# Kernel tuning notes

Hardware: AMD Instinct MI355X
Metric: run time of the kernel (lower is better)

Reference implementation:

```python
import jax, jax.numpy as jnp
import numpy as np

TOP_K = 2  # config.moe_config['moe_top_k']


def setup_inputs() -> dict:
    key = jax.random.key(0)
    k1, k2, k3, k4 = jax.random.split(key, 4)
    B, S, H, F, E = 2, 1024, 1024, 2048, 8
    def init(k, shape, fan_in):
        return jax.random.normal(k, shape, jnp.float32) / np.float32(np.sqrt(fan_in))
    return {
        "hidden_states": jax.random.normal(k1, (B, S, H), jnp.float32),
        "router_w": init(k2, (H, E), H),          # Linear(hidden, E, bias=False)
        "W1": init(k3, (E, H, 2 * F), H),          # per-expert Linear(hidden, 2*ffn)
        "W2": init(k4, (E, F, H), F),              # per-expert Linear(ffn, hidden)
    }


def reference(hidden_states, router_w, W1, W2):
    B, S, H = hidden_states.shape
    E = router_w.shape[1]
    x = hidden_states.reshape(-1, H)                      # [N, H], N = B*S
    N = x.shape[0]

    # router: logits -> fp32 softmax -> top-k -> renormalize (matches torch)
    logits = x @ router_w                                  # [N, E]
    probs = jax.nn.softmax(logits.astype(jnp.float32), axis=-1)
    rw, sel = jax.lax.top_k(probs, TOP_K)                  # [N, k]
    rw = rw / rw.sum(axis=-1, keepdims=True)
    rw = rw.astype(x.dtype)

    # combine weights per (token, expert); top-k experts are distinct so add==set
    cw = jnp.zeros((N, E), x.dtype).at[jnp.arange(N)[:, None], sel].add(rw)

    # per-expert SwiGLU MLP over all tokens, masked combine (full-capacity MoE)
    h = jnp.einsum('nh,ehf->enf', x, W1)                   # [E, N, 2F]
    a, b = jnp.split(h, 2, axis=-1)                        # gate, value halves
    g = jax.nn.silu(a) * b                                 # [E, N, F]
    y = jnp.einsum('enf,efh->enh', g, W2)                  # [E, N, H]
    out = jnp.einsum('enh,ne->nh', y, cw)                  # weighted scatter-combine
    return out.reshape(B, S, H)
```

## Files before the change

kernel.cpp:

```cpp
#include <hip/hip_runtime.h>
#include <hip/hip_bf16.h>

#define H_DIM 1024
#define E_NUM 8
#define F_DIM 2048
#define N_TOK 2048
typedef unsigned int uint;
typedef short bf16x8 __attribute__((ext_vector_type(8)));
typedef float f32x4 __attribute__((ext_vector_type(4)));

#define WS_CNT   0
#define WS_LIST  256
#define WS_W     (WS_LIST + 8*N_TOK*4)
#define WS_G     131072
#define WS_Y     (WS_G + 4096*2048*2)
#define WS_XB    WS_Y


static __device__ __forceinline__ uint f2bf(float f) {
    uint u = __builtin_bit_cast(uint, f);
    return (u + 0x7FFFu + ((u >> 16) & 1u)) >> 16;
}
static __device__ __forceinline__ float bflo(uint u) { return __builtin_bit_cast(float, u << 16); }
static __device__ __forceinline__ float bfhi(uint u) { return __builtin_bit_cast(float, u & 0xFFFF0000u); }
static __device__ __forceinline__ uint cvtpk(float a, float b) {
    uint r;
    asm("v_cvt_pk_bf16_f32 %0, %1, %2" : "=v"(r) : "v"(a), "v"(b));
    return r;
}
static __device__ __forceinline__ void gload_lds16(const void* g, void* l) {
    __builtin_amdgcn_global_load_lds(
        (const __attribute__((address_space(1))) unsigned int*)g,
        (__attribute__((address_space(3))) unsigned int*)l,
        16, 0, 0);
}

__global__ __launch_bounds__(256) void cvt_x_kernel(const float* __restrict__ x,
                                                    unsigned short* __restrict__ xb)
{
    int c = blockIdx.x * 256 + threadIdx.x;
    int row = c >> 7, b = c & 127;
    int t = b >> 3, s = b & 7;
    int klo = t*64 + (s >> 2)*32 + (s & 3)*4;
    const float* xr = x + (size_t)row * H_DIM;
    float4 lo = *(const float4*)(xr + klo);
    float4 hi = *(const float4*)(xr + klo + 16);
    uint4 o;
    o.x = cvtpk(lo.x, lo.y); o.y = cvtpk(lo.z, lo.w);
    o.z = cvtpk(hi.x, hi.y); o.w = cvtpk(hi.z, hi.w);
    *(uint4*)(xb + (size_t)row * H_DIM + b*8) = o;
}

__global__ __launch_bounds__(256) void router_kernel(
    const float* __restrict__ x, const float* __restrict__ rw,
    int* __restrict__ cnt, int* __restrict__ list, float* __restrict__ w_entry)
{
    int wave = threadIdx.x >> 6, lane = threadIdx.x & 63;
    int n = blockIdx.x * 4 + wave;
    const float* xr = x + (size_t)n * H_DIM;
    float acc[8] = {0,0,0,0,0,0,0,0};
    #pragma unroll
    for (int i = 0; i < H_DIM/64; ++i) {
        int h = i*64 + lane;
        float xv = xr[h];
        const float4* rr = (const float4*)(rw + (size_t)h*8);
        float4 r0 = rr[0], r1 = rr[1];
        acc[0] += xv*r0.x; acc[1] += xv*r0.y; acc[2] += xv*r0.z; acc[3] += xv*r0.w;
        acc[4] += xv*r1.x; acc[5] += xv*r1.y; acc[6] += xv*r1.z; acc[7] += xv*r1.w;
    }
    #pragma unroll
    for (int e = 0; e < 8; ++e) {
        float v = acc[e];
        #pragma unroll
        for (int off = 32; off; off >>= 1) v += __shfl_xor(v, off);
        acc[e] = v;
    }
    int e0 = 0;
    #pragma unroll
    for (int e = 1; e < 8; ++e) if (acc[e] > acc[e0]) e0 = e;
    int e1 = -1;
    #pragma unroll
    for (int e = 0; e < 8; ++e) if (e != e0 && (e1 < 0 || acc[e] > acc[e1])) e1 = e;
    float w0 = 1.0f / (1.0f + __expf(acc[e1] - acc[e0]));
    float w1 = 1.0f - w0;
    if (lane == 0) {
        int p0 = atomicAdd(&cnt[e0], 1);
        list[e0*N_TOK + p0] = n*2;
        w_entry[n*2] = w0;
        int p1 = atomicAdd(&cnt[e1], 1);
        list[e1*N_TOK + p1] = n*2 + 1;
        w_entry[n*2+1] = w1;
    }
}

template<int IS_G1>
__global__ __launch_bounds__(256, 4) void moe_gemm_kernel(
    const unsigned short* __restrict__ Asrc, const float* __restrict__ W,
    const int* __restrict__ cnt, const int* __restrict__ list,
    const float* __restrict__ w_entry, unsigned short* __restrict__ dst)
{
    constexpr int KTOT  = IS_G1 ? H_DIM : F_DIM;
    constexpr int BLD   = IS_G1 ? 2*F_DIM : H_DIM;
    constexpr int DLD   = IS_G1 ? F_DIM : H_DIM;
    constexpr int ALD   = IS_G1 ? H_DIM : F_DIM;
    constexpr int NMT   = 32;
    constexpr int NNT   = IS_G1 ? 32 : 16;
    constexpr int BSROW = IS_G1 ? 512 : 256;
    constexpr int NBS   = IS_G1 ? 4 : 2;
    constexpr int NM    = IS_G1 ? 4 : 2;
    constexpr int NT    = KTOT / 64;

    __shared__ __align__(16) unsigned short As[2][64*64];
    __shared__ __align__(16) uint Bs[32*BSROW/4];
    __shared__ int   s_entry[64];
    __shared__ float s_wrow[64];

    constexpr int nb = NMT * NNT * E_NUM;
    constexpr int chunk = nb >> 3;
    int bid = blockIdx.x;
    int f  = (bid & 7) * chunk + (bid >> 3);
    int mt = f % NMT;
    int nt = (f / NMT) % NNT;
    int e  = f / (NMT * NNT);

    const int c = cnt[e];
    if (mt * 64 >= c) return;
    const int tid = threadIdx.x;

    if (tid < 64) {
        int r = mt*64 + tid;
        int rr = r < c ? r : c - 1;
        int ent = list[e*N_TOK + rr];
        s_entry[tid] = ent;
        if constexpr (!IS_G1) s_wrow[tid] = w_entry[ent];
    }
    __syncthreads();

    const int lane = tid & 63, wid = tid >> 6;
    const int l15 = lane & 15, lg = lane >> 4;
    const int wr = IS_G1 ? 0 : (wid >> 1);
    const int wc = wid & 1;
    const int rowbase = IS_G1 ? 0 : wr*32;

    const unsigned short* a_src[2];
    #pragma unroll
    for (int i = 0; i < 2; ++i) {
        int sl  = wid*2048 + i*1024 + lane*16;
        int row = sl >> 7;
        int kb  = ((sl >> 4) & 7) ^ (row & 7);
        int ent = s_entry[row];
        int arow = IS_G1 ? (ent >> 1) : ent;
        a_src[i] = Asrc + (size_t)arow * ALD + kb*8;
    }

    const float* Wb = W + (size_t)e * (size_t)(IS_G1 ? H_DIM*2*F_DIM : F_DIM*H_DIM);
    const float* b_src[NBS]; int b_dst[NBS];
    #pragma unroll
    for (int s = 0; s < NBS; ++s) {
        int q = tid + s*256;
        int kp, c4, gc;
        if constexpr (IS_G1) {
            kp = q >> 5; c4 = q & 31;
            gc = (c4 < 16) ? (nt*64 + 4*c4) : (F_DIM + nt*64 + 4*(c4-16));
        } else {
            kp = q >> 4; c4 = q & 15;
            gc = nt*64 + 4*c4;
        }
        b_src[s] = Wb + (size_t)(2*kp) * BLD + gc;
        b_dst[s] = (kp*BSROW + c4*16) ^ ((kp & 4) << 4);
    }

    int a_addr[NM][2];
    #pragma unroll
    for (int m = 0; m < NM; ++m)
        #pragma unroll
        for (int kk = 0; kk < 2; ++kk) {
            int row = rowbase + m*16 + l15;
            a_addr[m][kk] = row*128 + ((kk*64 + lg*16) ^ ((row & 7) << 4));
        }
    int b_base[2][2];
    const int xorv = ((2*lg) & 4) << 4;
    #pragma unroll
    for (int j = 0; j < 2; ++j) {
        int cb = IS_G1 ? (j ? (4 + wid) : wid) : (wc*2 + j);
        int co = ((cb*16 + l15) * 4) ^ xorv;
        #pragma unroll
        for (int kk = 0; kk < 2; ++kk)
            b_base[j][kk] = (kk*16 + 2*lg)*BSROW + co;
    }

    f32x4 acc[NM][2];
    #pragma unroll
    for (int m = 0; m < NM; ++m)
        #pragma unroll
        for (int j = 0; j < 2; ++j) acc[m][j] = (f32x4){0.f,0.f,0.f,0.f};

    auto compute_step = [&](const char* ab) {
        #pragma unroll
        for (int kk = 0; kk < 2; ++kk) {
            bf16x8 af[NM];
            #pragma unroll
            for (int m = 0; m < NM; ++m)
                af[m] = *(const bf16x8*)(ab + a_addr[m][kk]);
            bf16x8 bfr[2];
            #pragma unroll
            for (int j = 0; j < 2; ++j) {
                const char* bb = (const char*)Bs + b_base[j][kk];
                union { uint u[4]; bf16x8 v; } bu;
                bu.u[0] = *(const uint*)(bb);
                bu.u[1] = *(const uint*)(bb + BSROW);
                bu.u[2] = *(const uint*)(bb + 8*BSROW);
                bu.u[3] = *(const uint*)(bb + 9*BSROW);
                bfr[j] = bu.v;
            }
            #pragma unroll
            for (int m = 0; m < NM; ++m)
                #pragma unroll
                for (int j = 0; j < 2; ++j)
                    acc[m][j] = __builtin_amdgcn_mfma_f32_16x16x32_bf16(af[m], bfr[j], acc[m][j], 0, 0, 0);
        }
    };

    #pragma unroll
    for (int i = 0; i < 2; ++i)
        gload_lds16(a_src[i], (char*)As[0] + wid*2048 + i*1024);
    {
        float4 r0[NBS], r1[NBS];
        #pragma unroll
        for (int s = 0; s < NBS; ++s) {
            r0[s] = *(const float4*)(b_src[s]);
            r1[s] = *(const float4*)(b_src[s] + BLD);
        }
        #pragma unroll
        for (int s = 0; s < NBS; ++s) {
            uint4 w4;
            w4.x = cvtpk(r0[s].x, r1[s].x); w4.y = cvtpk(r0[s].y, r1[s].y);
            w4.z = cvtpk(r0[s].z, r1[s].z); w4.w = cvtpk(r0[s].w, r1[s].w);
            *(uint4*)((char*)Bs + b_dst[s]) = w4;
        }
    }
    __syncthreads();

    for (int t = 0; t < NT; ++t) {
        float4 r0[NBS], r1[NBS];
        const bool more = (t + 1 < NT);
        if (more) {
            #pragma unroll
            for (int i = 0; i < 2; ++i)
                gload_lds16(a_src[i] + (t+1)*64, (char*)As[(t+1) & 1] + wid*2048 + i*1024);
            #pragma unroll
            for (int s = 0; s < NBS; ++s) {
                const float* b0 = b_src[s] + (size_t)(t+1) * 64 * BLD;
                r0[s] = *(const float4*)b0;
                r1[s] = *(const float4*)(b0 + BLD);
            }
        }
        compute_step((const char*)As[t & 1]);
        __syncthreads();
        if (more) {
            #pragma unroll
            for (int s = 0; s < NBS; ++s) {
                uint4 w4;
                w4.x = cvtpk(r0[s].x, r1[s].x); w4.y = cvtpk(r0[s].y, r1[s].y);
                w4.z = cvtpk(r0[s].z, r1[s].z); w4.w = cvtpk(r0[s].w, r1[s].w);
                *(uint4*)((char*)Bs + b_dst[s]) = w4;
            }
            __syncthreads();
        }
    }

    if constexpr (IS_G1) {
        const int pbase = nt*64 + ((wid >> 1)*4 + (l15 >> 2))*8 + (wid & 1)*4 + (l15 & 3);
        #pragma unroll
        for (int m = 0; m < NM; ++m) {
            f32x4 ga = acc[m][0], gv = acc[m][1];
            #pragma unroll
            for (int i = 0; i < 4; ++i) {
                int rl = m*16 + lg*4 + i;
                if (mt*64 + rl < c) {
                    int ent = s_entry[rl];
                    float a = ga[i];
                    float g = (a / (1.f + __expf(-a))) * gv[i];
                    dst[(size_t)ent * DLD + pbase] = (unsigned short)f2bf(g);
                }
            }
        }
    } else {
        #pragma unroll
        for (int m = 0; m < NM; ++m)
            #pragma unroll
            for (int j = 0; j < 2; ++j) {
                #pragma unroll
                for (int i = 0; i < 4; ++i) {
                    int rl = rowbase + m*16 + lg*4 + i;
                    if (mt*64 + rl < c) {
                        int ent = s_entry[rl];
                        float v = s_wrow[rl] * acc[m][j][i];
                        int col = nt*64 + wc*32 + j*16 + l15;
                        dst[(size_t)ent * DLD + col] = (unsigned short)f2bf(v);
                    }
                }
            }
    }
}

__global__ __launch_bounds__(256) void combine_kernel(
    const unsigned short* __restrict__ y, float* __restrict__ out)
{
    int gid = blockIdx.x * 256 + threadIdx.x;
    size_t base = (size_t)gid * 8;
    int n = (int)(base >> 10), h = (int)(base & 1023);
    const uint4 a = *(const uint4*)(y + (size_t)(2*n)   * 1024 + h);
    const uint4 b = *(const uint4*)(y + (size_t)(2*n+1) * 1024 + h);
    float4 o0, o1;
    o0.x = bflo(a.x)+bflo(b.x); o0.y = bfhi(a.x)+bfhi(b.x);
    o0.z = bflo(a.y)+bflo(b.y); o0.w = bfhi(a.y)+bfhi(b.y);
    o1.x = bflo(a.z)+bflo(b.z); o1.y = bfhi(a.z)+bfhi(b.z);
    o1.z = bflo(a.w)+bflo(b.w); o1.w = bfhi(a.w)+bfhi(b.w);
    *(float4*)(out + base)     = o0;
    *(float4*)(out + base + 4) = o1;
}

extern "C" void kernel_launch(void* const* d_in, const int* in_sizes, int n_in,
                              void* d_out, int out_size, void* d_ws, size_t ws_size,
                              hipStream_t stream) {
    const float* x  = (const float*)d_in[0];
    const float* rw = (const float*)d_in[1];
    const float* W1 = (const float*)d_in[2];
    const float* W2 = (const float*)d_in[3];
    float* out = (float*)d_out;
    char* ws = (char*)d_ws;
    int*   cnt     = (int*)(ws + WS_CNT);
    int*   list    = (int*)(ws + WS_LIST);
    float* w_entry = (float*)(ws + WS_W);
    unsigned short* g  = (unsigned short*)(ws + WS_G);
    unsigned short* y  = (unsigned short*)(ws + WS_Y);
    unsigned short* xb = (unsigned short*)(ws + WS_XB);

    hipMemsetAsync(cnt, 0, E_NUM * sizeof(int), stream);
    cvt_x_kernel<<<N_TOK*H_DIM/2048, 256, 0, stream>>>(x, xb);
    router_kernel<<<N_TOK/4, 256, 0, stream>>>(x, rw, cnt, list, w_entry);
    moe_gemm_kernel<1><<<32*32*E_NUM, 256, 0, stream>>>(xb, W1, cnt, list, w_entry, g);
    moe_gemm_kernel<0><<<32*16*E_NUM, 256, 0, stream>>>(g,  W2, cnt, list, w_entry, y);
    combine_kernel<<<(out_size/8 + 255)/256, 256, 0, stream>>>(y, out);
}
```

Measured before the change: 207.5 us.

## Stream fp32 weights directly into LDS with async loads and double-buffer both operands

The MoE GEMM kernel now loads fp32 weight tiles straight into LDS through global_load_lds and converts them to bf16 at fragment-read time, replacing the register round-trip and the separate LDS store. Both the A and B tiles are double-buffered with a two-stage prefetch, and explicit vmcnt waits plus barriers replace the per-iteration syncthreads pairs. The second GEMM is reshaped to 64x128 tiles so both GEMMs share one 4-wave layout, and the token list and weights are read from global memory instead of being staged in shared memory. LDS use grows and occupancy is lowered to 2 blocks per SM. The weight conversion is also repeated on every fragment read instead of once per tile.

```diff
diff --git a/kernel.cpp b/kernel.cpp
--- a/kernel.cpp
+++ b/kernel.cpp
@@ -33,6 +33,10 @@
         (const __attribute__((address_space(1))) unsigned int*)g,
         (__attribute__((address_space(3))) unsigned int*)l,
         16, 0, 0);
+}
+template<int N> static __device__ __forceinline__ void vmwait() {
+    if constexpr (N == 0)       asm volatile("s_waitcnt vmcnt(0)" ::: "memory");
+    else if constexpr (N == 10) asm volatile("s_waitcnt vmcnt(10)" ::: "memory");
 }
 
 __global__ __launch_bounds__(256) void cvt_x_kernel(const float* __restrict__ x,
@@ -94,7 +98,7 @@
 }
 
 template<int IS_G1>
-__global__ __launch_bounds__(256, 4) void moe_gemm_kernel(
+__global__ __launch_bounds__(256, 2) void moe_gemm_kernel(
     const unsigned short* __restrict__ Asrc, const float* __restrict__ W,
     const int* __restrict__ cnt, const int* __restrict__ list,
     const float* __restrict__ w_entry, unsigned short* __restrict__ dst)
@@ -104,16 +108,11 @@
     constexpr int DLD   = IS_G1 ? F_DIM : H_DIM;
     constexpr int ALD   = IS_G1 ? H_DIM : F_DIM;
     constexpr int NMT   = 32;
-    constexpr int NNT   = IS_G1 ? 32 : 16;
-    constexpr int BSROW = IS_G1 ? 512 : 256;
-    constexpr int NBS   = IS_G1 ? 4 : 2;
-    constexpr int NM    = IS_G1 ? 4 : 2;
+    constexpr int NNT   = IS_G1 ? 32 : 8;
     constexpr int NT    = KTOT / 64;
 
     __shared__ __align__(16) unsigned short As[2][64*64];
-    __shared__ __align__(16) uint Bs[32*BSROW/4];
-    __shared__ int   s_entry[64];
-    __shared__ float s_wrow[64];
+    __shared__ __align__(16) uint Bs[2][64*128];
 
     constexpr int nb = NMT * NNT * E_NUM;
     constexpr int chunk = nb >> 3;
@@ -126,21 +125,9 @@
     const int c = cnt[e];
     if (mt * 64 >= c) return;
     const int tid = threadIdx.x;
-
-    if (tid < 64) {
-        int r = mt*64 + tid;
-        int rr = r < c ? r : c - 1;
-        int ent = list[e*N_TOK + rr];
-        s_entry[tid] = ent;
-        if constexpr (!IS_G1) s_wrow[tid] = w_entry[ent];
-    }
-    __syncthreads();
-
     const int lane = tid & 63, wid = tid >> 6;
     const int l15 = lane & 15, lg = lane >> 4;
-    const int wr = IS_G1 ? 0 : (wid >> 1);
-    const int wc = wid & 1;
-    const int rowbase = IS_G1 ? 0 : wr*32;
+    const int lbase = e * N_TOK + mt * 64;
 
     const unsigned short* a_src[2];
     #pragma unroll
@@ -148,137 +135,118 @@
         int sl  = wid*2048 + i*1024 + lane*16;
         int row = sl >> 7;
         int kb  = ((sl >> 4) & 7) ^ (row & 7);
-        int ent = s_entry[row];
+        int rr  = (mt*64 + row) < c ? row : (c - 1 - mt*64);
+        int ent = list[lbase + rr];
         int arow = IS_G1 ? (ent >> 1) : ent;
         a_src[i] = Asrc + (size_t)arow * ALD + kb*8;
     }
 
     const float* Wb = W + (size_t)e * (size_t)(IS_G1 ? H_DIM*2*F_DIM : F_DIM*H_DIM);
-    const float* b_src[NBS]; int b_dst[NBS];
-    #pragma unroll
-    for (int s = 0; s < NBS; ++s) {
-        int q = tid + s*256;
-        int kp, c4, gc;
-        if constexpr (IS_G1) {
-            kp = q >> 5; c4 = q & 31;
-            gc = (c4 < 16) ? (nt*64 + 4*c4) : (F_DIM + nt*64 + 4*(c4-16));
-        } else {
-            kp = q >> 4; c4 = q & 15;
-            gc = nt*64 + 4*c4;
-        }
-        b_src[s] = Wb + (size_t)(2*kp) * BLD + gc;
-        b_dst[s] = (kp*BSROW + c4*16) ^ ((kp & 4) << 4);
-    }
-
-    int a_addr[NM][2];
-    #pragma unroll
-    for (int m = 0; m < NM; ++m)
+    const float* b_srcp[8];
+    #pragma unroll
+    for (int i = 0; i < 8; ++i) {
+        int k  = wid*16 + i*2 + (lane >> 5);
+        int c4 = (lane & 31) ^ (k & 12);
+        int gc;
+        if constexpr (IS_G1) gc = (c4 < 16) ? (nt*64 + 4*c4) : (F_DIM + nt*64 + 4*(c4-16));
+        else                 gc = nt*128 + 4*c4;
+        b_srcp[i] = Wb + (size_t)k * BLD + gc;
+    }
+
+    int a_addr[4][2];
+    #pragma unroll
+    for (int m = 0; m < 4; ++m)
         #pragma unroll
         for (int kk = 0; kk < 2; ++kk) {
-            int row = rowbase + m*16 + l15;
+            int row = m*16 + l15;
             a_addr[m][kk] = row*128 + ((kk*64 + lg*16) ^ ((row & 7) << 4));
         }
-    int b_base[2][2];
-    const int xorv = ((2*lg) & 4) << 4;
+    int b_base[2];
     #pragma unroll
     for (int j = 0; j < 2; ++j) {
-        int cb = IS_G1 ? (j ? (4 + wid) : wid) : (wc*2 + j);
-        int co = ((cb*16 + l15) * 4) ^ xorv;
-        #pragma unroll
-        for (int kk = 0; kk < 2; ++kk)
-            b_base[j][kk] = (kk*16 + 2*lg)*BSROW + co;
-    }
-
-    f32x4 acc[NM][2];
-    #pragma unroll
-    for (int m = 0; m < NM; ++m)
+        int cb = j ? (4 + wid) : wid;
+        b_base[j] = ((cb*16 + l15) * 4) ^ (lg << 6);
+    }
+
+    f32x4 acc[4][2];
+    #pragma unroll
+    for (int m = 0; m < 4; ++m)
         #pragma unroll
         for (int j = 0; j < 2; ++j) acc[m][j] = (f32x4){0.f,0.f,0.f,0.f};
 
-    auto compute_step = [&](const char* ab) {
+    auto STAGE = [&](int tt) {
+        const int b = tt & 1;
+        #pragma unroll
+        for (int i = 0; i < 2; ++i)
+            gload_lds16(a_src[i] + tt*64, (char*)As[b] + wid*2048 + i*1024);
+        #pragma unroll
+        for (int i = 0; i < 8; ++i)
+            gload_lds16(b_srcp[i] + (size_t)tt * 64 * BLD, (char*)Bs[b] + wid*8192 + i*1024);
+    };
+
+    auto compute_step = [&](const char* ab, const char* bb0) {
         #pragma unroll
         for (int kk = 0; kk < 2; ++kk) {
-            bf16x8 af[NM];
-            #pragma unroll
-            for (int m = 0; m < NM; ++m)
+            bf16x8 af[4];
+            #pragma unroll
+            for (int m = 0; m < 4; ++m)
                 af[m] = *(const bf16x8*)(ab + a_addr[m][kk]);
             bf16x8 bfr[2];
             #pragma unroll
             for (int j = 0; j < 2; ++j) {
-                const char* bb = (const char*)Bs + b_base[j][kk];
+                const char* bb = bb0 + (kk*32 + 4*lg)*512 + b_base[j];
+                float fA0 = *(const float*)(bb);
+                float fA1 = *(const float*)(bb + 512);
+                float fA2 = *(const float*)(bb + 1024);
+                float fA3 = *(const float*)(bb + 1536);
+                float fB0 = *(const float*)(bb + 8192);
+                float fB1 = *(const float*)(bb + 8192 + 512);
+                float fB2 = *(const float*)(bb + 8192 + 1024);
+                float fB3 = *(const float*)(bb + 8192 + 1536);
                 union { uint u[4]; bf16x8 v; } bu;
-                bu.u[0] = *(const uint*)(bb);
-                bu.u[1] = *(const uint*)(bb + BSROW);
-                bu.u[2] = *(const uint*)(bb + 8*BSROW);
-                bu.u[3] = *(const uint*)(bb + 9*BSROW);
+                bu.u[0] = cvtpk(fA0, fA1);
+                bu.u[1] = cvtpk(fA2, fA3);
+                bu.u[2] = cvtpk(fB0, fB1);
+                bu.u[3] = cvtpk(fB2, fB3);
                 bfr[j] = bu.v;
             }
             #pragma unroll
-            for (int m = 0; m < NM; ++m)
+            for (int m = 0; m < 4; ++m)
                 #pragma unroll
                 for (int j = 0; j < 2; ++j)
                     acc[m][j] = __builtin_amdgcn_mfma_f32_16x16x32_bf16(af[m], bfr[j], acc[m][j], 0, 0, 0);
         }
     };
 
-    #pragma unroll
-    for (int i = 0; i < 2; ++i)
-        gload_lds16(a_src[i], (char*)As[0] + wid*2048 + i*1024);
-    {
-        float4 r0[NBS], r1[NBS];
-        #pragma unroll
-        for (int s = 0; s < NBS; ++s) {
-            r0[s] = *(const float4*)(b_src[s]);
-            r1[s] = *(const float4*)(b_src[s] + BLD);
-        }
-        #pragma unroll
-        for (int s = 0; s < NBS; ++s) {
-            uint4 w4;
-            w4.x = cvtpk(r0[s].x, r1[s].x); w4.y = cvtpk(r0[s].y, r1[s].y);
-            w4.z = cvtpk(r0[s].z, r1[s].z); w4.w = cvtpk(r0[s].w, r1[s].w);
-            *(uint4*)((char*)Bs + b_dst[s]) = w4;
-        }
-    }
-    __syncthreads();
-
+    STAGE(0);
+    STAGE(1);
+
+    #pragma unroll
     for (int t = 0; t < NT; ++t) {
-        float4 r0[NBS], r1[NBS];
-        const bool more = (t + 1 < NT);
-        if (more) {
-            #pragma unroll
-            for (int i = 0; i < 2; ++i)
-                gload_lds16(a_src[i] + (t+1)*64, (char*)As[(t+1) & 1] + wid*2048 + i*1024);
-            #pragma unroll
-            for (int s = 0; s < NBS; ++s) {
-                const float* b0 = b_src[s] + (size_t)(t+1) * 64 * BLD;
-                r0[s] = *(const float4*)b0;
-                r1[s] = *(const float4*)(b0 + BLD);
-            }
-        }
-        compute_step((const char*)As[t & 1]);
-        __syncthreads();
-        if (more) {
-            #pragma unroll
-            for (int s = 0; s < NBS; ++s) {
-                uint4 w4;
-                w4.x = cvtpk(r0[s].x, r1[s].x); w4.y = cvtpk(r0[s].y, r1[s].y);
-                w4.z = cvtpk(r0[s].z, r1[s].z); w4.w = cvtpk(r0[s].w, r1[s].w);
-                *(uint4*)((char*)Bs + b_dst[s]) = w4;
-            }
-            __syncthreads();
+        if (t < NT - 1) vmwait<10>();
+        else            vmwait<0>();
+        __builtin_amdgcn_sched_barrier(0);
+        __builtin_amdgcn_s_barrier();
+        asm volatile("" ::: "memory");
+        compute_step((const char*)As[t & 1], (const char*)Bs[t & 1]);
+        if (t + 2 < NT) {
+            asm volatile("" ::: "memory");
+            __builtin_amdgcn_s_barrier();
+            asm volatile("" ::: "memory");
+            STAGE(t + 2);
         }
     }
 
     if constexpr (IS_G1) {
         const int pbase = nt*64 + ((wid >> 1)*4 + (l15 >> 2))*8 + (wid & 1)*4 + (l15 & 3);
         #pragma unroll
-        for (int m = 0; m < NM; ++m) {
+        for (int m = 0; m < 4; ++m) {
             f32x4 ga = acc[m][0], gv = acc[m][1];
             #pragma unroll
             for (int i = 0; i < 4; ++i) {
                 int rl = m*16 + lg*4 + i;
                 if (mt*64 + rl < c) {
-                    int ent = s_entry[rl];
+                    int ent = list[lbase + rl];
                     float a = ga[i];
                     float g = (a / (1.f + __expf(-a))) * gv[i];
                     dst[(size_t)ent * DLD + pbase] = (unsigned short)f2bf(g);
@@ -287,17 +255,17 @@
         }
     } else {
         #pragma unroll
-        for (int m = 0; m < NM; ++m)
-            #pragma unroll
-            for (int j = 0; j < 2; ++j) {
-                #pragma unroll
-                for (int i = 0; i < 4; ++i) {
-                    int rl = rowbase + m*16 + lg*4 + i;
-                    if (mt*64 + rl < c) {
-                        int ent = s_entry[rl];
-                        float v = s_wrow[rl] * acc[m][j][i];
-                        int col = nt*64 + wc*32 + j*16 + l15;
-                        dst[(size_t)ent * DLD + col] = (unsigned short)f2bf(v);
+        for (int m = 0; m < 4; ++m)
+            #pragma unroll
+            for (int i = 0; i < 4; ++i) {
+                int rl = m*16 + lg*4 + i;
+                if (mt*64 + rl < c) {
+                    int ent = list[lbase + rl];
+                    float w = w_entry[ent];
+                    #pragma unroll
+                    for (int j = 0; j < 2; ++j) {
+                        int col = nt*128 + (j ? (64 + wid*16) : (wid*16)) + l15;
+                        dst[(size_t)ent * DLD + col] = (unsigned short)f2bf(w * acc[m][j][i]);
                     }
                 }
             }
@@ -341,6 +309,6 @@
     cvt_x_kernel<<<N_TOK*H_DIM/2048, 256, 0, stream>>>(x, xb);
     router_kernel<<<N_TOK/4, 256, 0, stream>>>(x, rw, cnt, list, w_entry);
     moe_gemm_kernel<1><<<32*32*E_NUM, 256, 0, stream>>>(xb, W1, cnt, list, w_entry, g);
-    moe_gemm_kernel<0><<<32*16*E_NUM, 256, 0, stream>>>(g,  W2, cnt, list, w_entry, y);
+    moe_gemm_kernel<0><<<32*8*E_NUM, 256, 0, stream>>>(g,  W2, cnt, list, w_entry, y);
     combine_kernel<<<(out_size/8 + 255)/256, 256, 0, stream>>>(y, out);
 }
```

Result: slower. 254.2 us (+22.5%).

## Gather routed tokens contiguously and double-buffer weight tiles in MoE GEMMs

Applied to the files above, without the earlier changes.

Replaces the dense x-to-bf16 conversion with a prefix-sum plus gather kernel that writes each expert's routed tokens contiguously in bf16. The GEMMs then read A rows directly instead of going through an index indirection, and the G1 output is stored in that expert-sorted order. The main loop is rebuilt with double-buffered 32-row B sub-tiles in LDS, explicit vmcnt/lgkmcnt waits and barriers, to overlap global weight loads with MFMA work. It also raises the G2 occupancy hint and looks up the routing weights per row in the epilogue. The cost is two extra small kernel launches and a more fragile hand-written wait schedule.

```diff
diff --git a/kernel.cpp b/kernel.cpp
--- a/kernel.cpp
+++ b/kernel.cpp
@@ -10,11 +10,12 @@
 typedef float f32x4 __attribute__((ext_vector_type(4)));
 
 #define WS_CNT   0
+#define WS_OFF   64
 #define WS_LIST  256
 #define WS_W     (WS_LIST + 8*N_TOK*4)
 #define WS_G     131072
-#define WS_Y     (WS_G + 4096*2048*2)
-#define WS_XB    WS_Y
+#define WS_AX    (WS_G + 4096*2048*2)
+#define WS_Y     WS_AX
 
 
 static __device__ __forceinline__ uint f2bf(float f) {
@@ -34,21 +35,16 @@
         (__attribute__((address_space(3))) unsigned int*)l,
         16, 0, 0);
 }
-
-__global__ __launch_bounds__(256) void cvt_x_kernel(const float* __restrict__ x,
-                                                    unsigned short* __restrict__ xb)
-{
-    int c = blockIdx.x * 256 + threadIdx.x;
-    int row = c >> 7, b = c & 127;
-    int t = b >> 3, s = b & 7;
-    int klo = t*64 + (s >> 2)*32 + (s & 3)*4;
-    const float* xr = x + (size_t)row * H_DIM;
-    float4 lo = *(const float4*)(xr + klo);
-    float4 hi = *(const float4*)(xr + klo + 16);
-    uint4 o;
-    o.x = cvtpk(lo.x, lo.y); o.y = cvtpk(lo.z, lo.w);
-    o.z = cvtpk(hi.x, hi.y); o.w = cvtpk(hi.z, hi.w);
-    *(uint4*)(xb + (size_t)row * H_DIM + b*8) = o;
+template<int N> static __device__ __forceinline__ void vmwait() {
+    if constexpr (N == 0)      asm volatile("s_waitcnt vmcnt(0)" ::: "memory");
+    else if constexpr (N == 2) asm volatile("s_waitcnt vmcnt(2)" ::: "memory");
+    else if constexpr (N == 4) asm volatile("s_waitcnt vmcnt(4)" ::: "memory");
+}
+static __device__ __forceinline__ void lgk0_bar() {
+    asm volatile("s_waitcnt lgkmcnt(0)" ::: "memory");
+    __builtin_amdgcn_sched_barrier(0);
+    __builtin_amdgcn_s_barrier();
+    asm volatile("" ::: "memory");
 }
 
 __global__ __launch_bounds__(256) void router_kernel(
@@ -93,27 +89,61 @@
     }
 }
 
+__global__ void prefix_kernel(const int* __restrict__ cnt, int* __restrict__ off) {
+    if (threadIdx.x == 0) {
+        int s = 0;
+        #pragma unroll
+        for (int e = 0; e < E_NUM; ++e) { off[e] = s; s += cnt[e]; }
+        off[E_NUM] = s;
+    }
+}
+
+__global__ __launch_bounds__(256) void gather_kernel(
+    const float* __restrict__ x, const int* __restrict__ cnt, const int* __restrict__ off,
+    const int* __restrict__ list, unsigned short* __restrict__ Ax)
+{
+    int e = blockIdx.x >> 9;
+    int r = (blockIdx.x & 511)*4 + (threadIdx.x >> 6);
+    int lane = threadIdx.x & 63;
+    if (r >= cnt[e]) return;
+    int ent = list[e*N_TOK + r];
+    const float* xr = x + (size_t)(ent >> 1) * H_DIM;
+    unsigned short* dr = Ax + (size_t)(off[e] + r) * H_DIM;
+    #pragma unroll
+    for (int q = 0; q < 2; ++q) {
+        int b = lane*2 + q;
+        int t = b >> 3, s = b & 7;
+        int klo = t*64 + (s >> 2)*32 + (s & 3)*4;
+        float4 lo = *(const float4*)(xr + klo);
+        float4 hi = *(const float4*)(xr + klo + 16);
+        uint4 o;
+        o.x = cvtpk(lo.x, lo.y); o.y = cvtpk(lo.z, lo.w);
+        o.z = cvtpk(hi.x, hi.y); o.w = cvtpk(hi.z, hi.w);
+        *(uint4*)(dr + b*8) = o;
+    }
+}
+
 template<int IS_G1>
-__global__ __launch_bounds__(256, 4) void moe_gemm_kernel(
+__global__ __launch_bounds__(256, IS_G1 ? 4 : 5) void moe_gemm_kernel(
     const unsigned short* __restrict__ Asrc, const float* __restrict__ W,
-    const int* __restrict__ cnt, const int* __restrict__ list,
-    const float* __restrict__ w_entry, unsigned short* __restrict__ dst)
+    const int* __restrict__ cnt, const int* __restrict__ off,
+    const int* __restrict__ list, const float* __restrict__ w_entry,
+    unsigned short* __restrict__ dst)
 {
     constexpr int KTOT  = IS_G1 ? H_DIM : F_DIM;
     constexpr int BLD   = IS_G1 ? 2*F_DIM : H_DIM;
     constexpr int DLD   = IS_G1 ? F_DIM : H_DIM;
     constexpr int ALD   = IS_G1 ? H_DIM : F_DIM;
+    constexpr int ROWS  = 64;
+    constexpr int NM    = IS_G1 ? 4 : 2;
     constexpr int NMT   = 32;
     constexpr int NNT   = IS_G1 ? 32 : 16;
     constexpr int BSROW = IS_G1 ? 512 : 256;
-    constexpr int NBS   = IS_G1 ? 4 : 2;
-    constexpr int NM    = IS_G1 ? 4 : 2;
-    constexpr int NT    = KTOT / 64;
-
-    __shared__ __align__(16) unsigned short As[2][64*64];
-    __shared__ __align__(16) uint Bs[32*BSROW/4];
-    __shared__ int   s_entry[64];
-    __shared__ float s_wrow[64];
+    constexpr int NBS   = IS_G1 ? 2 : 1;
+    constexpr int NT2   = KTOT / 64;
+
+    __shared__ __align__(16) unsigned short As[2][ROWS*64];
+    __shared__ __align__(16) uint Bs[2][16*BSROW/4];
 
     constexpr int nb = NMT * NNT * E_NUM;
     constexpr int chunk = nb >> 3;
@@ -124,18 +154,9 @@
     int e  = f / (NMT * NNT);
 
     const int c = cnt[e];
-    if (mt * 64 >= c) return;
+    if (mt * ROWS >= c) return;
+    const int abase = off[e] + mt * ROWS;
     const int tid = threadIdx.x;
-
-    if (tid < 64) {
-        int r = mt*64 + tid;
-        int rr = r < c ? r : c - 1;
-        int ent = list[e*N_TOK + rr];
-        s_entry[tid] = ent;
-        if constexpr (!IS_G1) s_wrow[tid] = w_entry[ent];
-    }
-    __syncthreads();
-
     const int lane = tid & 63, wid = tid >> 6;
     const int l15 = lane & 15, lg = lane >> 4;
     const int wr = IS_G1 ? 0 : (wid >> 1);
@@ -148,9 +169,8 @@
         int sl  = wid*2048 + i*1024 + lane*16;
         int row = sl >> 7;
         int kb  = ((sl >> 4) & 7) ^ (row & 7);
-        int ent = s_entry[row];
-        int arow = IS_G1 ? (ent >> 1) : ent;
-        a_src[i] = Asrc + (size_t)arow * ALD + kb*8;
+        int gr  = abase + row; gr = gr < 4095 ? gr : 4095;
+        a_src[i] = Asrc + (size_t)gr * ALD + kb*8;
     }
 
     const float* Wb = W + (size_t)e * (size_t)(IS_G1 ? H_DIM*2*F_DIM : F_DIM*H_DIM);
@@ -174,19 +194,16 @@
     #pragma unroll
     for (int m = 0; m < NM; ++m)
         #pragma unroll
-        for (int kk = 0; kk < 2; ++kk) {
+        for (int p = 0; p < 2; ++p) {
             int row = rowbase + m*16 + l15;
-            a_addr[m][kk] = row*128 + ((kk*64 + lg*16) ^ ((row & 7) << 4));
-        }
-    int b_base[2][2];
+            a_addr[m][p] = row*128 + ((p*64 + lg*16) ^ ((row & 7) << 4));
+        }
+    int b_base[2];
     const int xorv = ((2*lg) & 4) << 4;
     #pragma unroll
     for (int j = 0; j < 2; ++j) {
         int cb = IS_G1 ? (j ? (4 + wid) : wid) : (wc*2 + j);
-        int co = ((cb*16 + l15) * 4) ^ xorv;
-        #pragma unroll
-        for (int kk = 0; kk < 2; ++kk)
-            b_base[j][kk] = (kk*16 + 2*lg)*BSROW + co;
+        b_base[j] = (2*lg)*BSROW + (((cb*16 + l15) * 4) ^ xorv);
     }
 
     f32x4 acc[NM][2];
@@ -195,78 +212,79 @@
         #pragma unroll
         for (int j = 0; j < 2; ++j) acc[m][j] = (f32x4){0.f,0.f,0.f,0.f};
 
-    auto compute_step = [&](const char* ab) {
-        #pragma unroll
-        for (int kk = 0; kk < 2; ++kk) {
-            bf16x8 af[NM];
-            #pragma unroll
-            for (int m = 0; m < NM; ++m)
-                af[m] = *(const bf16x8*)(ab + a_addr[m][kk]);
-            bf16x8 bfr[2];
-            #pragma unroll
-            for (int j = 0; j < 2; ++j) {
-                const char* bb = (const char*)Bs + b_base[j][kk];
-                union { uint u[4]; bf16x8 v; } bu;
-                bu.u[0] = *(const uint*)(bb);
-                bu.u[1] = *(const uint*)(bb + BSROW);
-                bu.u[2] = *(const uint*)(bb + 8*BSROW);
-                bu.u[3] = *(const uint*)(bb + 9*BSROW);
-                bfr[j] = bu.v;
-            }
-            #pragma unroll
-            for (int m = 0; m < NM; ++m)
-                #pragma unroll
-                for (int j = 0; j < 2; ++j)
-                    acc[m][j] = __builtin_amdgcn_mfma_f32_16x16x32_bf16(af[m], bfr[j], acc[m][j], 0, 0, 0);
-        }
+    struct BQ { float4 r0[NBS], r1[NBS]; };
+    auto loadB = [&](int t) {
+        BQ q;
+        #pragma unroll
+        for (int s = 0; s < NBS; ++s) {
+            const float* p = b_src[s] + (size_t)t * 32 * BLD;
+            q.r0[s] = *(const float4*)p;
+            q.r1[s] = *(const float4*)(p + BLD);
+        }
+        return q;
     };
-
-    #pragma unroll
-    for (int i = 0; i < 2; ++i)
-        gload_lds16(a_src[i], (char*)As[0] + wid*2048 + i*1024);
-    {
-        float4 r0[NBS], r1[NBS];
-        #pragma unroll
-        for (int s = 0; s < NBS; ++s) {
-            r0[s] = *(const float4*)(b_src[s]);
-            r1[s] = *(const float4*)(b_src[s] + BLD);
-        }
+    auto dswB = [&](const BQ& q, int buf) {
         #pragma unroll
         for (int s = 0; s < NBS; ++s) {
             uint4 w4;
-            w4.x = cvtpk(r0[s].x, r1[s].x); w4.y = cvtpk(r0[s].y, r1[s].y);
-            w4.z = cvtpk(r0[s].z, r1[s].z); w4.w = cvtpk(r0[s].w, r1[s].w);
-            *(uint4*)((char*)Bs + b_dst[s]) = w4;
-        }
-    }
-    __syncthreads();
-
-    for (int t = 0; t < NT; ++t) {
-        float4 r0[NBS], r1[NBS];
-        const bool more = (t + 1 < NT);
-        if (more) {
+            w4.x = cvtpk(q.r0[s].x, q.r1[s].x); w4.y = cvtpk(q.r0[s].y, q.r1[s].y);
+            w4.z = cvtpk(q.r0[s].z, q.r1[s].z); w4.w = cvtpk(q.r0[s].w, q.r1[s].w);
+            *(uint4*)((char*)Bs[buf] + b_dst[s]) = w4;
+        }
+    };
+    auto STAGE_A = [&](int a) {
+        #pragma unroll
+        for (int i = 0; i < 2; ++i)
+            gload_lds16(a_src[i] + a*64, (char*)As[a & 1] + wid*2048 + i*1024);
+    };
+    auto compute = [&](int P, int abuf) {
+        const char* ab  = (const char*)As[abuf];
+        const char* bb0 = (const char*)Bs[P];
+        bf16x8 bfr[2];
+        #pragma unroll
+        for (int j = 0; j < 2; ++j) {
+            const char* bb = bb0 + b_base[j];
+            union { uint u[4]; bf16x8 v; } bu;
+            bu.u[0] = *(const uint*)(bb);
+            bu.u[1] = *(const uint*)(bb + BSROW);
+            bu.u[2] = *(const uint*)(bb + 8*BSROW);
+            bu.u[3] = *(const uint*)(bb + 9*BSROW);
+            bfr[j] = bu.v;
+        }
+        #pragma unroll
+        for (int m = 0; m < NM; ++m) {
+            bf16x8 af = *(const bf16x8*)(ab + (P ? a_addr[m][1] : a_addr[m][0]));
             #pragma unroll
-            for (int i = 0; i < 2; ++i)
-                gload_lds16(a_src[i] + (t+1)*64, (char*)As[(t+1) & 1] + wid*2048 + i*1024);
-            #pragma unroll
-            for (int s = 0; s < NBS; ++s) {
-                const float* b0 = b_src[s] + (size_t)(t+1) * 64 * BLD;
-                r0[s] = *(const float4*)b0;
-                r1[s] = *(const float4*)(b0 + BLD);
-            }
-        }
-        compute_step((const char*)As[t & 1]);
-        __syncthreads();
-        if (more) {
-            #pragma unroll
-            for (int s = 0; s < NBS; ++s) {
-                uint4 w4;
-                w4.x = cvtpk(r0[s].x, r1[s].x); w4.y = cvtpk(r0[s].y, r1[s].y);
-                w4.z = cvtpk(r0[s].z, r1[s].z); w4.w = cvtpk(r0[s].w, r1[s].w);
-                *(uint4*)((char*)Bs + b_dst[s]) = w4;
-            }
-            __syncthreads();
-        }
+            for (int j = 0; j < 2; ++j)
+                acc[m][j] = __builtin_amdgcn_mfma_f32_16x16x32_bf16(af, bfr[j], acc[m][j], 0, 0, 0);
+        }
+    };
+
+    STAGE_A(0);
+    { BQ q0 = loadB(0); dswB(q0, 0); }
+    BQ qW = loadB(1);
+    BQ qN;
+
+    for (int tp = 0; tp < NT2 - 1; ++tp) {
+        vmwait<2*NBS>(); __builtin_amdgcn_sched_barrier(0);
+        lgk0_bar();
+        STAGE_A(tp + 1);
+        qN = loadB(2*tp + 2);
+        compute(0, tp & 1);
+        dswB(qW, 1);
+        lgk0_bar();
+        qW = loadB(2*tp + 3);
+        compute(1, tp & 1);
+        dswB(qN, 0);
+    }
+    {
+        const int ab = (NT2 - 1) & 1;
+        vmwait<2*NBS>(); __builtin_amdgcn_sched_barrier(0);
+        lgk0_bar();
+        compute(0, ab);
+        dswB(qW, 1);
+        lgk0_bar();
+        compute(1, ab);
     }
 
     if constexpr (IS_G1) {
@@ -277,27 +295,27 @@
             #pragma unroll
             for (int i = 0; i < 4; ++i) {
                 int rl = m*16 + lg*4 + i;
-                if (mt*64 + rl < c) {
-                    int ent = s_entry[rl];
+                if (mt*ROWS + rl < c) {
                     float a = ga[i];
                     float g = (a / (1.f + __expf(-a))) * gv[i];
-                    dst[(size_t)ent * DLD + pbase] = (unsigned short)f2bf(g);
+                    dst[(size_t)(abase + rl) * DLD + pbase] = (unsigned short)f2bf(g);
                 }
             }
         }
     } else {
+        const int lbase = e * N_TOK + mt * ROWS;
         #pragma unroll
         for (int m = 0; m < NM; ++m)
             #pragma unroll
-            for (int j = 0; j < 2; ++j) {
-                #pragma unroll
-                for (int i = 0; i < 4; ++i) {
-                    int rl = rowbase + m*16 + lg*4 + i;
-                    if (mt*64 + rl < c) {
-                        int ent = s_entry[rl];
-                        float v = s_wrow[rl] * acc[m][j][i];
+            for (int i = 0; i < 4; ++i) {
+                int rl = rowbase + m*16 + lg*4 + i;
+                if (mt*ROWS + rl < c) {
+                    int ent = list[lbase + rl];
+                    float w = w_entry[ent];
+                    #pragma unroll
+                    for (int j = 0; j < 2; ++j) {
                         int col = nt*64 + wc*32 + j*16 + l15;
-                        dst[(size_t)ent * DLD + col] = (unsigned short)f2bf(v);
+                        dst[(size_t)ent * DLD + col] = (unsigned short)f2bf(w * acc[m][j][i]);
                     }
                 }
             }
@@ -331,16 +349,18 @@
     float* out = (float*)d_out;
     char* ws = (char*)d_ws;
     int*   cnt     = (int*)(ws + WS_CNT);
+    int*   off     = (int*)(ws + WS_OFF);
     int*   list    = (int*)(ws + WS_LIST);
     float* w_entry = (float*)(ws + WS_W);
     unsigned short* g  = (unsigned short*)(ws + WS_G);
+    unsigned short* Ax = (unsigned short*)(ws + WS_AX);
     unsigned short* y  = (unsigned short*)(ws + WS_Y);
-    unsigned short* xb = (unsigned short*)(ws + WS_XB);
 
     hipMemsetAsync(cnt, 0, E_NUM * sizeof(int), stream);
-    cvt_x_kernel<<<N_TOK*H_DIM/2048, 256, 0, stream>>>(x, xb);
     router_kernel<<<N_TOK/4, 256, 0, stream>>>(x, rw, cnt, list, w_entry);
-    moe_gemm_kernel<1><<<32*32*E_NUM, 256, 0, stream>>>(xb, W1, cnt, list, w_entry, g);
-    moe_gemm_kernel<0><<<32*16*E_NUM, 256, 0, stream>>>(g,  W2, cnt, list, w_entry, y);
+    prefix_kernel<<<1, 64, 0, stream>>>(cnt, off);
+    gather_kernel<<<E_NUM*512, 256, 0, stream>>>(x, cnt, off, list, Ax);
+    moe_gemm_kernel<1><<<32*32*E_NUM, 256, 0, stream>>>(Ax, W1, cnt, off, list, w_entry, g);
+    moe_gemm_kernel<0><<<32*16*E_NUM, 256, 0, stream>>>(g,  W2, cnt, off, list, w_entry, y);
     combine_kernel<<<(out_size/8 + 255)/256, 256, 0, stream>>>(y, out);
 }
```

New measurement: 203.6 us (median of 2 runs). Within noise of the previous version (-1.9%).
